# Kernel tuning notes

Hardware: AMD Instinct MI355X
Metric: run time of the kernel (lower is better)

The kernel has to match this reference:

```python
import jax, jax.numpy as jnp
import numpy as np

B, S, MEM, L, E, H = 8, 512, 512, 4, 512, 8
DH = E // H
OBS = 128
K = MEM + S


def setup_inputs() -> dict:
    key = jax.random.key(0)
    ks = jax.random.split(key, 16)
    def w(k, shape, s=0.02):
        return jax.random.normal(k, shape, jnp.float32) * s
    # causal-with-memory mask: query i may attend to kv positions j <= MEM + i
    mask = jnp.arange(K)[None, None, None, :] <= (MEM + jnp.arange(S))[None, None, :, None]
    return {
        "obs": w(ks[0], (B, S, OBS), 1.0),
        "memories": w(ks[1], (B, MEM, L, E), 1.0),
        "mask": mask,
        "W_enc": w(ks[2], (OBS, E)), "b_enc": jnp.zeros((E,), jnp.float32),
        "ln1_s": jnp.ones((L, E), jnp.float32), "ln1_b": jnp.zeros((L, E), jnp.float32),
        "Wq": w(ks[3], (L, E, H, DH)), "bq": jnp.zeros((L, H, DH), jnp.float32),
        "Wk": w(ks[4], (L, E, H, DH)), "bk": jnp.zeros((L, H, DH), jnp.float32),
        "Wv": w(ks[5], (L, E, H, DH)), "bv": jnp.zeros((L, H, DH), jnp.float32),
        "Wr": w(ks[6], (L, E, H, DH)),
        "u_bias": w(ks[7], (L, H, DH)), "v_bias": w(ks[8], (L, H, DH)),
        "Wo": w(ks[9], (L, H, DH, E)), "bo": jnp.zeros((L, E), jnp.float32),
        "ln2_s": jnp.ones((L, E), jnp.float32), "ln2_b": jnp.zeros((L, E), jnp.float32),
        "W1": w(ks[10], (L, E, E)), "b1": jnp.zeros((L, E), jnp.float32),
        "W2": w(ks[11], (L, E, E)), "b2": jnp.zeros((L, E), jnp.float32),
    }


def _ln(x, s, b, eps=1e-6):
    m = x.mean(-1, keepdims=True)
    v = ((x - m) ** 2).mean(-1, keepdims=True)
    return (x - m) * jax.lax.rsqrt(v + eps) * s + b


def _rel_shift(x):
    # Transformer-XL relative shift: [B,H,Q,Kk] -> shifted [B,H,Q,Kk]
    b, h, q, k = x.shape
    x = jnp.pad(x, ((0, 0), (0, 0), (0, 0), (1, 0)))
    return x.reshape(b, h, k + 1, q)[:, :, 1:, :].reshape(b, h, q, k)


def _forward(obs, memories, mask, W_enc, b_enc, ln1_s, ln1_b, Wq, bq, Wk, bk, Wv, bv,
             Wr, u_bias, v_bias, Wo, bo, ln2_s, ln2_b, W1, b1, W2, b2):
    x = obs @ W_enc + b_enc  # [B,S,E]
    klen = memories.shape[1] + x.shape[1]
    e = x.shape[-1]
    # PositionalEmbedding: pos_seq = [klen, klen-1, ..., 1]
    inv_freq = 1.0 / (10000.0 ** (jnp.arange(0, e, 2, dtype=jnp.float32) / e))
    sin_inp = jnp.outer(jnp.arange(klen, 0, -1, dtype=jnp.float32), inv_freq)
    pe = jnp.concatenate([jnp.sin(sin_inp), jnp.cos(sin_inp)], axis=-1)  # [K,E]
    scale = 1.0 / jnp.sqrt(jnp.asarray(Wq.shape[-1], jnp.float32))
    for i in range(Wq.shape[0]):
        mem_cat = jnp.concatenate([memories[:, :, i], x], axis=1)  # [B,K,E]
        vk = _ln(mem_cat, ln1_s[i], ln1_b[i])
        qn = _ln(x, ln1_s[i], ln1_b[i])
        q = jnp.einsum('bse,ehd->bshd', qn, Wq[i]) + bq[i]
        k = jnp.einsum('bke,ehd->bkhd', vk, Wk[i]) + bk[i]
        vv = jnp.einsum('bke,ehd->bkhd', vk, Wv[i]) + bv[i]
        r = jnp.einsum('ke,ehd->khd', pe, Wr[i])
        ac = jnp.einsum('bqhd,bkhd->bhqk', q + u_bias[i], k)     # content term
        bd = _rel_shift(jnp.einsum('bqhd,khd->bhqk', q + v_bias[i], r))  # position term
        scores = jnp.where(mask, (ac + bd) * scale, jnp.float32(-1e30))
        attn = jax.nn.softmax(scores, axis=-1)
        o = jnp.einsum('bhqk,bkhd->bqhd', attn, vv)
        attn_out = jnp.einsum('bqhd,hde->bqe', o, Wo[i]) + bo[i]
        h = x + attn_out                      # residual (gating=False)
        hn = _ln(h, ln2_s[i], ln2_b[i])
        ff = jax.nn.gelu(hn @ W1[i] + b1[i]) @ W2[i] + b2[i]
        x = ff + h
    return x


def reference(obs, memories, mask, W_enc, b_enc, ln1_s, ln1_b, Wq, bq, Wk, bk, Wv, bv,
              Wr, u_bias, v_bias, Wo, bo, ln2_s, ln2_b, W1, b1, W2, b2):
    return _forward(obs, memories, mask, W_enc, b_enc, ln1_s, ln1_b, Wq, bq, Wk, bk,
                    Wv, bv, Wr, u_bias, v_bias, Wo, bo, ln2_s, ln2_b, W1, b1, W2, b2)
```

## Files before the change

### kernel.cpp

```cpp
#include <hip/hip_runtime.h>
#include <hip/hip_bf16.h>
#include <math.h>

#define B     8
#define S     512
#define MEM   512
#define L     4
#define E     512
#define H     8
#define DH    64
#define OBS   128
#define KLEN  1024
#define FQ    64
#define FK    64

typedef __hip_bfloat16 bf16;
using frag_ab = __attribute__((ext_vector_type(8))) short;
using frag_cd = __attribute__((ext_vector_type(4))) float;

__device__ __forceinline__ float gelu_tanh(float x) {
    return 0.5f * x * (1.0f + tanhf(0.7978845608028654f * (x + 0.044715f * x * x * x)));
}
__device__ __forceinline__ unsigned short f2bs(float x) {
    bf16 h = __float2bfloat16(x); return *(unsigned short*)&h;
}
__device__ __forceinline__ float bs2f(short s) {
    union { unsigned u; float f; } t; t.u = ((unsigned)(unsigned short)s) << 16; return t.f;
}

__global__ __launch_bounds__(256) void setup_kernel(
    const float* __restrict__ obs, bf16* __restrict__ obsb, bf16* __restrict__ pe)
{
    const int i = blockIdx.x * 256 + threadIdx.x;
    if (i < B * S * OBS) {
        obsb[i] = __float2bfloat16(obs[i]);
    } else {
        const int idx = i - B * S * OBS;
        const int p = idx >> 9;
        const int j = idx & 511;
        const float pos = (float)(KLEN - p);
        const int m = (j < 256) ? j : (j - 256);
        const float invf = expf(-(float)(2 * m) * (9.210340371976184f / (float)E));
        const float a = pos * invf;
        pe[idx] = __float2bfloat16((j < 256) ? sinf(a) : cosf(a));
    }
}

__global__ __launch_bounds__(256) void transpose_all_kernel(
    const float* __restrict__ Wq, const float* __restrict__ Wk,
    const float* __restrict__ Wv, const float* __restrict__ Wr,
    const float* __restrict__ Wo, const float* __restrict__ W1,
    const float* __restrict__ W2, const float* __restrict__ Wenc,
    bf16* __restrict__ WqT, bf16* __restrict__ WkvT, bf16* __restrict__ WrT,
    bf16* __restrict__ WoT, bf16* __restrict__ W1T, bf16* __restrict__ W2T,
    bf16* __restrict__ WencT)
{
    __shared__ float t[32][33];
    const int z = blockIdx.z;
    const int bn = blockIdx.x * 32, bk = blockIdx.y * 32;
    const int tx = threadIdx.x & 31, ty = threadIdx.x >> 5;
    if (z == 28) {
        if (blockIdx.y >= OBS / 32) return;
        #pragma unroll
        for (int r = 0; r < 32; r += 8)
            t[ty + r][tx] = Wenc[(size_t)(bk + ty + r) * E + bn + tx];
        __syncthreads();
        #pragma unroll
        for (int r = 0; r < 32; r += 8)
            WencT[(size_t)(bn + ty + r) * OBS + bk + tx] = __float2bfloat16(t[tx][ty + r]);
        return;
    }
    const int which = z >> 2, li = z & 3;
    const size_t so = (size_t)li * E * E;
    const float* src; bf16* dst;
    switch (which) {
        case 0: src = Wq + so; dst = WqT + so; break;
        case 1: src = Wk + so; dst = WkvT + (size_t)li * 2 * E * E; break;
        case 2: src = Wv + so; dst = WkvT + (size_t)li * 2 * E * E + (size_t)E * E; break;
        case 3: src = Wr + so; dst = WrT + so; break;
        case 4: src = Wo + so; dst = WoT + so; break;
        case 5: src = W1 + so; dst = W1T + so; break;
        default: src = W2 + so; dst = W2T + so; break;
    }
    #pragma unroll
    for (int r = 0; r < 32; r += 8)
        t[ty + r][tx] = src[(size_t)(bk + ty + r) * E + bn + tx];
    __syncthreads();
    #pragma unroll
    for (int r = 0; r < 32; r += 8)
        dst[(size_t)(bn + ty + r) * E + bk + tx] = __float2bfloat16(t[tx][ty + r]);
}

__device__ __forceinline__ void gemm_body(
    short* As, short* Bs,
    const bf16* __restrict__ A, const bf16* __restrict__ Bt,
    int m0, int n0, int K, int N,
    const float* bias, const float* bias_u, const float* bias_v,
    const float* res, float* Cf, bf16* Cb, bf16* Cb2, int act, int mode)
{
    const int tid = threadIdx.x;
    const int w = tid >> 6, lane = tid & 63;
    const int wm2 = (w >> 1) * 64, wn2 = (w & 1) * 32;
    const int fr = lane & 15, quad = lane >> 4;

    const int arow = tid >> 1, acol = (tid & 1) * 32;
    const int brow = tid >> 2, bcol = (tid & 3) * 16;
    const short* Ag = (const short*)A + (size_t)(m0 + arow) * K + acol;
    const short* Bg = (const short*)Bt + (size_t)(n0 + brow) * K + bcol;
    short* Asw = &As[arow * 72 + acol];
    short* Bsw = &Bs[brow * 72 + bcol];

    frag_cd acc[4][2];
    #pragma unroll
    for (int i = 0; i < 4; ++i)
        #pragma unroll
        for (int j = 0; j < 2; ++j)
            acc[i][j] = (frag_cd)(0.0f);

    uint4 a0 = *(const uint4*)(Ag);
    uint4 a1 = *(const uint4*)(Ag + 8);
    uint4 a2 = *(const uint4*)(Ag + 16);
    uint4 a3 = *(const uint4*)(Ag + 24);
    uint4 b0 = *(const uint4*)(Bg);
    uint4 b1 = *(const uint4*)(Bg + 8);

    for (int k0 = 0; k0 < K; k0 += 64) {
        __syncthreads();
        *(uint4*)(Asw) = a0; *(uint4*)(Asw + 8) = a1;
        *(uint4*)(Asw + 16) = a2; *(uint4*)(Asw + 24) = a3;
        *(uint4*)(Bsw) = b0; *(uint4*)(Bsw + 8) = b1;
        if (k0 + 64 < K) {
            a0 = *(const uint4*)(Ag + k0 + 64);
            a1 = *(const uint4*)(Ag + k0 + 72);
            a2 = *(const uint4*)(Ag + k0 + 80);
            a3 = *(const uint4*)(Ag + k0 + 88);
            b0 = *(const uint4*)(Bg + k0 + 64);
            b1 = *(const uint4*)(Bg + k0 + 72);
        }
        asm volatile("s_waitcnt lgkmcnt(0)" ::: "memory");
        __builtin_amdgcn_s_barrier();
        __builtin_amdgcn_sched_barrier(0);
        #pragma unroll
        for (int kh = 0; kh < 2; ++kh) {
            frag_ab af[4], bfr[2];
            #pragma unroll
            for (int i = 0; i < 4; ++i)
                af[i] = *(const frag_ab*)&As[(wm2 + i * 16 + fr) * 72 + kh * 32 + quad * 8];
            #pragma unroll
            for (int j = 0; j < 2; ++j)
                bfr[j] = *(const frag_ab*)&Bs[(wn2 + j * 16 + fr) * 72 + kh * 32 + quad * 8];
            #pragma unroll
            for (int i = 0; i < 4; ++i)
                #pragma unroll
                for (int j = 0; j < 2; ++j)
                    acc[i][j] = __builtin_amdgcn_mfma_f32_16x16x32_bf16(af[i], bfr[j], acc[i][j], 0, 0, 0);
        }
    }

    if (mode == 2 && n0 >= 512) {
        short* ts = As;
        __syncthreads();
        #pragma unroll
        for (int i = 0; i < 4; ++i) {
            #pragma unroll
            for (int r = 0; r < 4; ++r) {
                const int kl = wm2 + i * 16 + quad * 4 + r;
                #pragma unroll
                for (int j = 0; j < 2; ++j) {
                    const int dl = wn2 + j * 16 + fr;
                    ts[dl * 130 + kl] =
                        (short)f2bs(acc[i][j][r] + bias_v[(n0 - 512) + dl]);
                }
            }
        }
        __syncthreads();
        const int bb = m0 >> 10;
        const int kb = m0 & 1023;
        const int dl = tid >> 2;
        const int q4 = tid & 3;
        short vals[32];
        #pragma unroll
        for (int i2 = 0; i2 < 32; ++i2) {
            const int kp  = q4 * 32 + i2;
            const int kpl = kp & 63;
            const int src = (kp & 64) + (((kpl & 3) << 4) | (kpl >> 2));
            vals[i2] = ts[dl * 130 + src];
        }
        short* dst = (short*)Cb2 + ((size_t)(bb * E + (n0 - 512) + dl)) * KLEN
                   + kb + q4 * 32;
        *(uint4*)(dst)      = *(const uint4*)&vals[0];
        *(uint4*)(dst + 8)  = *(const uint4*)&vals[8];
        *(uint4*)(dst + 16) = *(const uint4*)&vals[16];
        *(uint4*)(dst + 24) = *(const uint4*)&vals[24];
        return;
    }

    #pragma unroll
    for (int i = 0; i < 4; ++i) {
        #pragma unroll
        for (int r = 0; r < 4; ++r) {
            const int m = m0 + wm2 + i * 16 + quad * 4 + r;
            #pragma unroll
            for (int j = 0; j < 2; ++j) {
                const int n = n0 + wn2 + j * 16 + fr;
                float v = acc[i][j][r];
                if (bias) v += bias[n];
                if (act)  v = gelu_tanh(v);
                if (res)  v += res[(size_t)m * N + n];
                if (mode == 2) {
                    Cb[(size_t)m * 512 + n] = __float2bfloat16(v + bias_u[n]);
                } else if (mode == 1) {
                    Cb[(size_t)m * N + n]  = __float2bfloat16((v + bias_u[n]) * 0.125f);
                    Cb2[(size_t)m * N + n] = __float2bfloat16((v + bias_v[n]) * 0.125f);
                } else {
                    if (Cf) Cf[(size_t)m * N + n] = v;
                    if (Cb) Cb[(size_t)m * N + n] = __float2bfloat16(v);
                }
            }
        }
    }
}

__device__ __forceinline__ void gemm64_body(
    short* As, short* Bs,
    const bf16* __restrict__ A, const bf16* __restrict__ Bt,
    int m0, int n0, int K, int N,
    const float* bias, const float* res, float* Cf, bf16* Cb, int act)
{
    const int tid = threadIdx.x;
    const int w = tid >> 6, lane = tid & 63;
    const int wm2 = (w >> 1) * 32, wn2 = (w & 1) * 32;
    const int fr = lane & 15, quad = lane >> 4;

    const int arow = tid >> 2, acol = (tid & 3) * 16;
    const short* Ag = (const short*)A + (size_t)(m0 + arow) * K + acol;
    const short* Bg = (const short*)Bt + (size_t)(n0 + arow) * K + acol;
    short* Asw = &As[arow * 72 + acol];
    short* Bsw = &Bs[arow * 72 + acol];

    frag_cd acc[2][2];
    #pragma unroll
    for (int i = 0; i < 2; ++i)
        #pragma unroll
        for (int j = 0; j < 2; ++j)
            acc[i][j] = (frag_cd)(0.0f);

    uint4 a0 = *(const uint4*)(Ag);
    uint4 a1 = *(const uint4*)(Ag + 8);
    uint4 b0 = *(const uint4*)(Bg);
    uint4 b1 = *(const uint4*)(Bg + 8);

    for (int k0 = 0; k0 < K; k0 += 64) {
        __syncthreads();
        *(uint4*)(Asw) = a0; *(uint4*)(Asw + 8) = a1;
        *(uint4*)(Bsw) = b0; *(uint4*)(Bsw + 8) = b1;
        if (k0 + 64 < K) {
            a0 = *(const uint4*)(Ag + k0 + 64);
            a1 = *(const uint4*)(Ag + k0 + 72);
            b0 = *(const uint4*)(Bg + k0 + 64);
            b1 = *(const uint4*)(Bg + k0 + 72);
        }
        asm volatile("s_waitcnt lgkmcnt(0)" ::: "memory");
        __builtin_amdgcn_s_barrier();
        __builtin_amdgcn_sched_barrier(0);
        #pragma unroll
        for (int kh = 0; kh < 2; ++kh) {
            frag_ab af[2], bfr[2];
            #pragma unroll
            for (int i = 0; i < 2; ++i)
                af[i] = *(const frag_ab*)&As[(wm2 + i * 16 + fr) * 72 + kh * 32 + quad * 8];
            #pragma unroll
            for (int j = 0; j < 2; ++j)
                bfr[j] = *(const frag_ab*)&Bs[(wn2 + j * 16 + fr) * 72 + kh * 32 + quad * 8];
            #pragma unroll
            for (int i = 0; i < 2; ++i)
                #pragma unroll
                for (int j = 0; j < 2; ++j)
                    acc[i][j] = __builtin_amdgcn_mfma_f32_16x16x32_bf16(af[i], bfr[j], acc[i][j], 0, 0, 0);
        }
    }

    #pragma unroll
    for (int i = 0; i < 2; ++i) {
        #pragma unroll
        for (int r = 0; r < 4; ++r) {
            const int m = m0 + wm2 + i * 16 + quad * 4 + r;
            #pragma unroll
            for (int j = 0; j < 2; ++j) {
                const int n = n0 + wn2 + j * 16 + fr;
                float v = acc[i][j][r];
                if (bias) v += bias[n];
                if (act)  v = gelu_tanh(v);
                if (res)  v += res[(size_t)m * N + n];
                if (Cf) Cf[(size_t)m * N + n] = v;
                if (Cb) Cb[(size_t)m * N + n] = __float2bfloat16(v);
            }
        }
    }
}

__global__ __launch_bounds__(256) void mfma_gemm_kernel(
    const bf16* __restrict__ A, const bf16* __restrict__ Bt,
    const float* __restrict__ bias, const float* __restrict__ res,
    float* __restrict__ Cf, bf16* __restrict__ Cb,
    int K, int N, int act)
{
    __shared__ short As[64 * 72];
    __shared__ short Bs[64 * 72];
    const int pid = blockIdx.x;
    const int swz = ((pid & 7) << 6) | (pid >> 3);
    gemm64_body(As, Bs, A, Bt, (swz >> 3) * 64, (swz & 7) * 64, K, N,
                bias, res, Cf, Cb, act);
}

__global__ __launch_bounds__(256) void qkvr_kernel(
    const bf16* __restrict__ QN, const bf16* __restrict__ VK,
    const bf16* __restrict__ PE_, const bf16* __restrict__ WqT,
    const bf16* __restrict__ WkvT, const bf16* __restrict__ WrT,
    const float* __restrict__ bq, const float* __restrict__ ub,
    const float* __restrict__ vbias, const float* __restrict__ bk,
    const float* __restrict__ bv,
    bf16* __restrict__ QU, bf16* __restrict__ QV,
    bf16* __restrict__ KB, bf16* __restrict__ VT, bf16* __restrict__ RB)
{
    __shared__ short As[128 * 72];
    __shared__ short Bs[64 * 72];
    const int bid = blockIdx.x;
    if (bid < 256) {
        const int swz = ((bid & 7) << 5) | (bid >> 3);
        gemm_body(As, Bs, QN, WqT, (swz >> 3) * 128, (swz & 7) * 64, E, E,
                  bq, ub, vbias, nullptr, nullptr, QU, QV, 0, 1);
    } else if (bid < 1280) {
        const int id = bid - 256;
        const int swz = ((id & 7) << 7) | (id >> 3);
        gemm_body(As, Bs, VK, WkvT, (swz >> 4) * 128, (swz & 15) * 64, E, 2 * E,
                  nullptr, bk, bv, nullptr, nullptr, KB, VT, 0, 2);
    } else {
        const int id = bid - 1280;
        const int swz = ((id & 7) << 3) | (id >> 3);
        gemm_body(As, Bs, PE_, WrT, (swz >> 3) * 128, (swz & 7) * 64, E, E,
                  nullptr, nullptr, nullptr, nullptr, nullptr, RB, nullptr, 0, 0);
    }
}

__global__ __launch_bounds__(256) void ln1_kernel(
    const float* __restrict__ mem, const float* __restrict__ X, int li,
    const float* __restrict__ gam, const float* __restrict__ bet,
    bf16* __restrict__ qn, bf16* __restrict__ vkdst)
{
    const int blk = blockIdx.x;
    const int t = threadIdx.x;
    const bool isMem = blk < B * MEM;
    const int rr = isMem ? blk : (blk - B * MEM);
    const float* sp = isMem ? (mem + ((size_t)rr * L + li) * E)
                            : (X + (size_t)rr * E);
    const float x0 = sp[t], x1 = sp[t + 256];
    float s = x0 + x1, ss = fmaf(x0, x0, x1 * x1);
    #pragma unroll
    for (int off = 32; off; off >>= 1) { s += __shfl_down(s, off, 64); ss += __shfl_down(ss, off, 64); }
    __shared__ float tmp[8];
    const int wid = t >> 6, lane = t & 63;
    if (!lane) { tmp[wid] = s; tmp[4 + wid] = ss; }
    __syncthreads();
    s = tmp[0] + tmp[1] + tmp[2] + tmp[3];
    ss = tmp[4] + tmp[5] + tmp[6] + tmp[7];
    const float mean = s * (1.0f / E);
    const float var = ss * (1.0f / E) - mean * mean;
    const float rstd = rsqrtf(var + 1e-6f);
    const float y0 = (x0 - mean) * rstd * gam[t] + bet[t];
    const float y1 = (x1 - mean) * rstd * gam[t + 256] + bet[t + 256];
    const int b = rr >> 9, p = rr & 511;
    if (isMem) {
        bf16* dst = vkdst + ((size_t)b * KLEN + p) * E;
        dst[t] = __float2bfloat16(y0); dst[t + 256] = __float2bfloat16(y1);
    } else {
        qn[(size_t)rr * E + t]       = __float2bfloat16(y0);
        qn[(size_t)rr * E + t + 256] = __float2bfloat16(y1);
        bf16* d2 = vkdst + ((size_t)b * KLEN + MEM + p) * E;
        d2[t] = __float2bfloat16(y0); d2[t + 256] = __float2bfloat16(y1);
    }
}

__global__ __launch_bounds__(256) void ln_f32_kernel(
    const float* __restrict__ src,
    const float* __restrict__ gam, const float* __restrict__ bet,
    bf16* __restrict__ dst1)
{
    const int rr = blockIdx.x;
    const int t = threadIdx.x;
    const float* sp = src + (size_t)rr * E;
    const float x0 = sp[t], x1 = sp[t + 256];
    float s = x0 + x1, ss = fmaf(x0, x0, x1 * x1);
    #pragma unroll
    for (int off = 32; off; off >>= 1) { s += __shfl_down(s, off, 64); ss += __shfl_down(ss, off, 64); }
    __shared__ float tmp[8];
    const int wid = t >> 6, lane = t & 63;
    if (!lane) { tmp[wid] = s; tmp[4 + wid] = ss; }
    __syncthreads();
    s = tmp[0] + tmp[1] + tmp[2] + tmp[3];
    ss = tmp[4] + tmp[5] + tmp[6] + tmp[7];
    const float mean = s * (1.0f / E);
    const float var = ss * (1.0f / E) - mean * mean;
    const float rstd = rsqrtf(var + 1e-6f);
    dst1[(size_t)rr * E + t]       = __float2bfloat16((x0 - mean) * rstd * gam[t] + bet[t]);
    dst1[(size_t)rr * E + t + 256] = __float2bfloat16((x1 - mean) * rstd * gam[t + 256] + bet[t + 256]);
}

__global__ __launch_bounds__(256) void mfma_flash_kernel(
    const bf16* __restrict__ Qu,
    const bf16* __restrict__ Qv,
    const bf16* __restrict__ Kb,
    const bf16* __restrict__ Vt,
    const bf16* __restrict__ Rb,
    bf16* __restrict__ O)
{
    const int pid = blockIdx.x;
    const int swz = ((pid & 7) << 6) | (pid >> 3);
    const int qphys = swz & 7;
    const int hb = swz >> 3;
    const int h = hb & 7, b = hb >> 3;
    const int qt = (qphys & 1) ? (7 - (qphys >> 1)) : (qphys >> 1);
    const int q0 = qt * FQ;
    const int t = threadIdx.x;
    const int w = t >> 6, lane = t & 63;
    const int fr = lane & 15, quad = lane >> 4;
    const int qbase = q0 + w * 16;

    __shared__ short Ks[64 * 64];
    __shared__ short Vs[64 * 64];
    __shared__ short Rs[128 * 64];
    __shared__ short BDs[4 * 80 * 18];
    __shared__ short Ps[4 * 16 * 64];

    const int fxk = fr & 7;
    const int xq0 = (quad ^ fxk) << 3;
    const int xq1 = ((quad + 4) ^ fxk) << 3;

    const short* quptr = (const short*)Qu + ((size_t)(b * S + qbase + fr)) * E + h * DH + quad * 8;
    const frag_ab au0 = *(const frag_ab*)(quptr);
    const frag_ab au1 = *(const frag_ab*)(quptr + 32);
    const short* qvptr = (const short*)Qv + ((size_t)(b * S + qbase + fr)) * E + h * DH + quad * 8;
    const frag_ab av0 = *(const frag_ab*)(qvptr);
    const frag_ab av1 = *(const frag_ab*)(qvptr + 32);

    frag_cd accO[4];
    #pragma unroll
    for (int i = 0; i < 4; ++i) accO[i] = (frag_cd)(0.0f);
    float mrow[4] = {-3.0e38f, -3.0e38f, -3.0e38f, -3.0e38f};
    float lrow[4] = {0.f, 0.f, 0.f, 0.f};

    const int srow = t >> 2, scol = (t & 3) * 16;
    const short* kg = (const short*)Kb + ((size_t)(b * KLEN + srow)) * E + h * DH + scol;
    const short* vg = (const short*)Vt + ((size_t)(b * E + h * DH + srow)) * KLEN + scol;
    const int sxs = srow & 7;
    const int scb = (t & 3) * 2;
    const int kvw0 = (srow << 6) + (((scb    ) ^ sxs) << 3);
    const int kvw1 = (srow << 6) + (((scb + 1) ^ sxs) << 3);
    const int ntb0 = 3 - w;
    const int b0 = 448 - q0;

    {
        const int rr = t >> 1, rc = (t & 1) * 32;
        const int j = b0 + rr;
        const int slot = j & 127;
        const int sx = slot & 7, cb = rc >> 3;
        const short* rp = (const short*)Rb + (size_t)j * E + h * DH + rc;
        *(uint4*)&Rs[(slot << 6) + (((cb    ) ^ sx) << 3)] = *(const uint4*)(rp);
        *(uint4*)&Rs[(slot << 6) + (((cb + 1) ^ sx) << 3)] = *(const uint4*)(rp + 8);
        *(uint4*)&Rs[(slot << 6) + (((cb + 2) ^ sx) << 3)] = *(const uint4*)(rp + 16);
        *(uint4*)&Rs[(slot << 6) + (((cb + 3) ^ sx) << 3)] = *(const uint4*)(rp + 24);
    }

    const int ntiles = 9 + qt;

    const int r64 = t >> 2, rc4 = (t & 3) * 16;
    uint4 ka0, ka1, va0, va1, ra0, ra1;
    int rslot = 0;
    {
        ka0 = *(const uint4*)(kg);
        ka1 = *(const uint4*)(kg + 8);
        va0 = *(const uint4*)(vg);
        va1 = *(const uint4*)(vg + 8);
    }

    for (int kt = 0; kt < ntiles; ++kt) {
        const int k0 = kt * FK;
        __syncthreads();
        {
            *(uint4*)&Ks[kvw0] = ka0;
            *(uint4*)&Ks[kvw1] = ka1;
            *(uint4*)&Vs[kvw0] = va0;
            *(uint4*)&Vs[kvw1] = va1;
        }
        if (kt >= 1) {
            const int sx = rslot & 7;
            *(uint4*)&Rs[(rslot << 6) + (((scb    ) ^ sx) << 3)] = ra0;
            *(uint4*)&Rs[(rslot << 6) + (((scb + 1) ^ sx) << 3)] = ra1;
        }
        if (kt + 1 < ntiles) {
            const short* kp = kg + (size_t)(k0 + FK) * E;
            ka0 = *(const uint4*)(kp);
            ka1 = *(const uint4*)(kp + 8);
            const short* vp = vg + k0 + FK;
            va0 = *(const uint4*)(vp);
            va1 = *(const uint4*)(vp + 8);
            int j = b0 + 64 * (kt + 1) + 64 + r64;
            rslot = j & 127;
            if (j > KLEN - 1) j = KLEN - 1;
            const short* rp = (const short*)Rb + (size_t)j * E + h * DH + rc4;
            ra0 = *(const uint4*)(rp);
            ra1 = *(const uint4*)(rp + 8);
        }
        asm volatile("s_waitcnt lgkmcnt(0)" ::: "memory");
        __builtin_amdgcn_s_barrier();
        __builtin_amdgcn_sched_barrier(0);

        const int roff = (b0 + 64 * kt) & 127;

        __builtin_amdgcn_s_setprio(1);
        #pragma unroll
        for (int i = 0; i < 5; ++i) {
            const int ntb = ntb0 + i;
            const int slot = (roff + ntb * 16 + fr) & 127;
            const frag_ab rf0 = *(const frag_ab*)&Rs[(slot << 6) + xq0];
            const frag_ab rf1 = *(const frag_ab*)&Rs[(slot << 6) + xq1];
            frag_cd z = (frag_cd)(0.0f);
            z = __builtin_amdgcn_mfma_f32_16x16x32_bf16(av0, rf0, z, 0, 0, 0);
            z = __builtin_amdgcn_mfma_f32_16x16x32_bf16(av1, rf1, z, 0, 0, 0);
            union { unsigned u[2]; unsigned short sh[4]; } pk;
            pk.sh[0] = f2bs(z[0]); pk.sh[1] = f2bs(z[1]);
            pk.sh[2] = f2bs(z[2]); pk.sh[3] = f2bs(z[3]);
            const int bdw = (w * 80 + i * 16 + fr) * 18 + quad * 4;
            *(unsigned*)&BDs[bdw]     = pk.u[0];
            *(unsigned*)&BDs[bdw + 2] = pk.u[1];
        }

        frag_cd sc[4];
        #pragma unroll
        for (int nt = 0; nt < 4; ++nt) {
            const int krow = (nt * 16 + fr) << 6;
            const frag_ab kf0 = *(const frag_ab*)&Ks[krow + xq0];
            const frag_ab kf1 = *(const frag_ab*)&Ks[krow + xq1];
            frag_cd z = (frag_cd)(0.0f);
            z = __builtin_amdgcn_mfma_f32_16x16x32_bf16(au0, kf0, z, 0, 0, 0);
            z = __builtin_amdgcn_mfma_f32_16x16x32_bf16(au1, kf1, z, 0, 0, 0);
            sc[nt] = z;
        }
        __builtin_amdgcn_s_setprio(0);

        const bool edge = (kt == ntiles - 1);
        #pragma unroll
        for (int r = 0; r < 4; ++r) {
            const int qw = quad * 4 + r;
            float sv[4];
            #pragma unroll
            for (int nt = 0; nt < 4; ++nt) {
                const int jlr = nt * 16 + fr + 15 - qw;
                const float bd = bs2f(BDs[(w * 80 + jlr) * 18 + qw]);
                sv[nt] = sc[nt][r] + bd;
            }
            if (edge) {
                const int qrow = qbase + qw;
                #pragma unroll
                for (int nt = 0; nt < 4; ++nt)
                    if (k0 + nt * 16 + fr > MEM + qrow) sv[nt] = -1e30f;
            }
            const float locmax = fmaxf(fmaxf(sv[0], sv[1]), fmaxf(sv[2], sv[3]));
            if (__any(locmax > mrow[r] + 4.0f)) {
                float tm = locmax;
                tm = fmaxf(tm, __shfl_xor(tm, 1, 64));
                tm = fmaxf(tm, __shfl_xor(tm, 2, 64));
                tm = fmaxf(tm, __shfl_xor(tm, 4, 64));
                tm = fmaxf(tm, __shfl_xor(tm, 8, 64));
                const float mn = fmaxf(mrow[r], tm);
                const float al = __expf(mrow[r] - mn);
                lrow[r] *= al;
                #pragma unroll
                for (int nt = 0; nt < 4; ++nt) accO[nt][r] *= al;
                mrow[r] = mn;
            }
            const float p0 = __expf(sv[0] - mrow[r]), p1 = __expf(sv[1] - mrow[r]);
            const float p2 = __expf(sv[2] - mrow[r]), p3 = __expf(sv[3] - mrow[r]);
            lrow[r] += (p0 + p1) + (p2 + p3);
            union { uint2 u2; unsigned short sh[4]; } pq;
            pq.sh[0] = f2bs(p0); pq.sh[1] = f2bs(p1);
            pq.sh[2] = f2bs(p2); pq.sh[3] = f2bs(p3);
            const int pw = (w << 10) + (qw << 6)
                         + (((fr >> 1) ^ (qw & 7)) << 3) + ((fr & 1) << 2);
            *(uint2*)&Ps[pw] = pq.u2;
        }

        const frag_ab pf0 = *(const frag_ab*)&Ps[(w << 10) + (fr << 6) + xq0];
        const frag_ab pf1 = *(const frag_ab*)&Ps[(w << 10) + (fr << 6) + xq1];
        __builtin_amdgcn_s_setprio(1);
        #pragma unroll
        for (int nt = 0; nt < 4; ++nt) {
            const int vrow = (nt * 16 + fr) << 6;
            const frag_ab vf0 = *(const frag_ab*)&Vs[vrow + xq0];
            const frag_ab vf1 = *(const frag_ab*)&Vs[vrow + xq1];
            accO[nt] = __builtin_amdgcn_mfma_f32_16x16x32_bf16(pf0, vf0, accO[nt], 0, 0, 0);
            accO[nt] = __builtin_amdgcn_mfma_f32_16x16x32_bf16(pf1, vf1, accO[nt], 0, 0, 0);
        }
        __builtin_amdgcn_s_setprio(0);
    }

    #pragma unroll
    for (int r = 0; r < 4; ++r) {
        float lsum = lrow[r];
        lsum += __shfl_xor(lsum, 1, 64);
        lsum += __shfl_xor(lsum, 2, 64);
        lsum += __shfl_xor(lsum, 4, 64);
        lsum += __shfl_xor(lsum, 8, 64);
        const float inv = 1.0f / lsum;
        bf16* po = O + ((size_t)(b * S + qbase + quad * 4 + r)) * E + h * DH + fr;
        #pragma unroll
        for (int nt = 0; nt < 4; ++nt)
            po[nt * 16] = __float2bfloat16(accO[nt][r] * inv);
    }
}

extern "C" void kernel_launch(void* const* d_in, const int* in_sizes, int n_in,
                              void* d_out, int out_size, void* d_ws, size_t ws_size,
                              hipStream_t stream)
{
    const float* obs  = (const float*)d_in[0];
    const float* mem  = (const float*)d_in[1];
    const float* Wenc = (const float*)d_in[3];
    const float* benc = (const float*)d_in[4];
    const float* ln1s = (const float*)d_in[5];
    const float* ln1b = (const float*)d_in[6];
    const float* Wq   = (const float*)d_in[7];
    const float* bq   = (const float*)d_in[8];
    const float* Wk   = (const float*)d_in[9];
    const float* bk   = (const float*)d_in[10];
    const float* Wv   = (const float*)d_in[11];
    const float* bv   = (const float*)d_in[12];
    const float* Wr   = (const float*)d_in[13];
    const float* ub   = (const float*)d_in[14];
    const float* vb   = (const float*)d_in[15];
    const float* Wo   = (const float*)d_in[16];
    const float* bo   = (const float*)d_in[17];
    const float* ln2s = (const float*)d_in[18];
    const float* ln2b = (const float*)d_in[19];
    const float* W1   = (const float*)d_in[20];
    const float* b1   = (const float*)d_in[21];
    const float* W2   = (const float*)d_in[22];
    const float* b2   = (const float*)d_in[23];

    float* wsf = (float*)d_ws;
    float* X = wsf;
    bf16* wsb = (bf16*)(wsf + (size_t)B * S * E);
    size_t ob = 0;
    bf16* OBSb = wsb + ob; ob += (size_t)B * S * OBS;
    bf16* QNb  = wsb + ob; ob += (size_t)B * S * E;
    bf16* PEb  = wsb + ob; ob += (size_t)KLEN * E;
    bf16* RBb  = wsb + ob; ob += (size_t)KLEN * E;
    bf16* WencT= wsb + ob; ob += (size_t)OBS * E;
    bf16* WqT  = wsb + ob; ob += (size_t)L * E * E;
    bf16* WkvT = wsb + ob; ob += (size_t)L * 2 * E * E;
    bf16* WrT  = wsb + ob; ob += (size_t)L * E * E;
    bf16* WoT  = wsb + ob; ob += (size_t)L * E * E;
    bf16* W1T  = wsb + ob; ob += (size_t)L * E * E;
    bf16* W2T  = wsb + ob; ob += (size_t)L * E * E;
    bf16* QUb  = wsb + ob; ob += (size_t)B * S * E;
    bf16* QVb  = wsb + ob; ob += (size_t)B * S * E;
    bf16* KBb  = wsb + ob; ob += (size_t)B * KLEN * E;
    bf16* VTb  = wsb + ob; ob += (size_t)B * E * KLEN;
    bf16* OBb  = wsb + ob; ob += (size_t)B * S * E;
    char* uni = (char*)(wsb + ob);
    bf16*  VKb = (bf16*)uni;
    float* HB  = (float*)uni;
    bf16*  FFb = (bf16*)(uni + ((size_t)8 << 20));


    transpose_all_kernel<<<dim3(E / 32, E / 32, 29), 256, 0, stream>>>(
        Wq, Wk, Wv, Wr, Wo, W1, W2, Wenc, WqT, WkvT, WrT, WoT, W1T, W2T, WencT);
    setup_kernel<<<(B * S * OBS + KLEN * E) / 256, 256, 0, stream>>>(obs, OBSb, PEb);

    mfma_gemm_kernel<<<512, 256, 0, stream>>>(
        OBSb, WencT, benc, nullptr, X, nullptr, OBS, E, 0);

    for (int li = 0; li < L; ++li) {
        const size_t wOff = (size_t)li * E * E;
        const size_t vOff = (size_t)li * E;

        ln1_kernel<<<2 * B * S, 256, 0, stream>>>(
            mem, X, li, ln1s + vOff, ln1b + vOff, QNb, VKb);

        qkvr_kernel<<<1344, 256, 0, stream>>>(
            QNb, VKb, PEb, WqT + wOff, WkvT + (size_t)li * 2 * E * E, WrT + wOff,
            bq + vOff, ub + vOff, vb + vOff, bk + vOff, bv + vOff,
            QUb, QVb, KBb, VTb, RBb);

        mfma_flash_kernel<<<512, 256, 0, stream>>>(
            QUb, QVb, KBb, VTb, RBb, OBb);

        mfma_gemm_kernel<<<512, 256, 0, stream>>>(
            OBb, WoT + wOff, bo + vOff, X, HB, nullptr, E, E, 0);
        ln_f32_kernel<<<B * S, 256, 0, stream>>>(HB, ln2s + vOff, ln2b + vOff, QNb);
        mfma_gemm_kernel<<<512, 256, 0, stream>>>(
            QNb, W1T + wOff, b1 + vOff, nullptr, nullptr, FFb, E, E, 1);
        float* dst = (li == L - 1) ? (float*)d_out : X;
        mfma_gemm_kernel<<<512, 256, 0, stream>>>(
            FFb, W2T + wOff, b2 + vOff, HB, dst, nullptr, E, E, 0);
    }
}
```

Baseline: 614.8 us.

## Fuse LayerNorm2 into Wo GEMM stats epilogue and W1 GEMM prologue

The Wo projection GEMM epilogue now accumulates per-row sum and sum-of-squares into a stats buffer via atomics, and a new W1 GEMM kernel applies the LayerNorm on the fly while loading f32 activations into shared memory. This removes the standalone ln_f32 kernel and its bf16 intermediate write/read each layer. Costs are atomic traffic, reading f32 instead of bf16 for the W1 A operand, and stats zeroing piggybacked on ln1_kernel. Variance is computed as E[x^2]-mean^2, which has slightly different numerics.

Result: faster. 580.9 us (median of 2 runs) (-5.5%).

```diff
diff --git a/kernel.cpp b/kernel.cpp
--- a/kernel.cpp
+++ b/kernel.cpp
@@ -225,7 +225,8 @@
     short* As, short* Bs,
     const bf16* __restrict__ A, const bf16* __restrict__ Bt,
     int m0, int n0, int K, int N,
-    const float* bias, const float* res, float* Cf, bf16* Cb, int act)
+    const float* bias, const float* res, float* Cf, bf16* Cb, int act,
+    float* stats)
 {
     const int tid = threadIdx.x;
     const int w = tid >> 6, lane = tid & 63;
@@ -285,6 +286,7 @@
         #pragma unroll
         for (int r = 0; r < 4; ++r) {
             const int m = m0 + wm2 + i * 16 + quad * 4 + r;
+            float s = 0.0f, sq = 0.0f;
             #pragma unroll
             for (int j = 0; j < 2; ++j) {
                 const int n = n0 + wn2 + j * 16 + fr;
@@ -294,6 +296,17 @@
                 if (res)  v += res[(size_t)m * N + n];
                 if (Cf) Cf[(size_t)m * N + n] = v;
                 if (Cb) Cb[(size_t)m * N + n] = __float2bfloat16(v);
+                s += v; sq = fmaf(v, v, sq);
+            }
+            if (stats) {
+                s  += __shfl_xor(s, 1, 64);  sq += __shfl_xor(sq, 1, 64);
+                s  += __shfl_xor(s, 2, 64);  sq += __shfl_xor(sq, 2, 64);
+                s  += __shfl_xor(s, 4, 64);  sq += __shfl_xor(sq, 4, 64);
+                s  += __shfl_xor(s, 8, 64);  sq += __shfl_xor(sq, 8, 64);
+                if (fr == 0) {
+                    atomicAdd(&stats[2 * m], s);
+                    atomicAdd(&stats[2 * m + 1], sq);
+                }
             }
         }
     }
@@ -303,14 +316,126 @@
     const bf16* __restrict__ A, const bf16* __restrict__ Bt,
     const float* __restrict__ bias, const float* __restrict__ res,
     float* __restrict__ Cf, bf16* __restrict__ Cb,
-    int K, int N, int act)
+    int K, int N, int act, float* stats)
 {
     __shared__ short As[64 * 72];
     __shared__ short Bs[64 * 72];
     const int pid = blockIdx.x;
     const int swz = ((pid & 7) << 6) | (pid >> 3);
     gemm64_body(As, Bs, A, Bt, (swz >> 3) * 64, (swz & 7) * 64, K, N,
-                bias, res, Cf, Cb, act);
+                bias, res, Cf, Cb, act, stats);
+}
+
+__global__ __launch_bounds__(256) void mfma_gemm_ln_kernel(
+    const float* __restrict__ A, const bf16* __restrict__ Bt,
+    const float* __restrict__ ST,
+    const float* __restrict__ gam, const float* __restrict__ bet,
+    const float* __restrict__ bias, bf16* __restrict__ Cb)
+{
+    __shared__ short As[64 * 72];
+    __shared__ short Bs[64 * 72];
+    __shared__ float gls[E], bls[E];
+    const int pid = blockIdx.x;
+    const int swz = ((pid & 7) << 6) | (pid >> 3);
+    const int m0 = (swz >> 3) * 64, n0 = (swz & 7) * 64;
+    const int tid = threadIdx.x;
+    *(float2*)&gls[tid * 2] = *(const float2*)&gam[tid * 2];
+    *(float2*)&bls[tid * 2] = *(const float2*)&bet[tid * 2];
+
+    const int w = tid >> 6, lane = tid & 63;
+    const int wm2 = (w >> 1) * 32, wn2 = (w & 1) * 32;
+    const int fr = lane & 15, quad = lane >> 4;
+
+    const int arow = tid >> 2, acol = (tid & 3) * 16;
+    const int g = m0 + arow;
+    const float mean = ST[2 * g] * (1.0f / E);
+    const float var  = ST[2 * g + 1] * (1.0f / E) - mean * mean;
+    const float rstd = rsqrtf(var + 1e-6f);
+    const float* Agf = A + (size_t)g * E + acol;
+    const short* Bg = (const short*)Bt + (size_t)(n0 + arow) * E + acol;
+    short* Asw = &As[arow * 72 + acol];
+    short* Bsw = &Bs[arow * 72 + acol];
+
+    frag_cd acc[2][2];
+    #pragma unroll
+    for (int i = 0; i < 2; ++i)
+        #pragma unroll
+        for (int j = 0; j < 2; ++j)
+            acc[i][j] = (frag_cd)(0.0f);
+
+    float4 f0 = *(const float4*)(Agf);
+    float4 f1 = *(const float4*)(Agf + 4);
+    float4 f2 = *(const float4*)(Agf + 8);
+    float4 f3 = *(const float4*)(Agf + 12);
+    uint4 b0 = *(const uint4*)(Bg);
+    uint4 b1 = *(const uint4*)(Bg + 8);
+
+    for (int k0 = 0; k0 < E; k0 += 64) {
+        __syncthreads();
+        {
+            const float* gp = &gls[k0 + acol];
+            const float* bp = &bls[k0 + acol];
+            union { uint4 u; unsigned short s[8]; } p0, p1;
+            p0.s[0] = f2bs((f0.x - mean) * rstd * gp[0]  + bp[0]);
+            p0.s[1] = f2bs((f0.y - mean) * rstd * gp[1]  + bp[1]);
+            p0.s[2] = f2bs((f0.z - mean) * rstd * gp[2]  + bp[2]);
+            p0.s[3] = f2bs((f0.w - mean) * rstd * gp[3]  + bp[3]);
+            p0.s[4] = f2bs((f1.x - mean) * rstd * gp[4]  + bp[4]);
+            p0.s[5] = f2bs((f1.y - mean) * rstd * gp[5]  + bp[5]);
+            p0.s[6] = f2bs((f1.z - mean) * rstd * gp[6]  + bp[6]);
+            p0.s[7] = f2bs((f1.w - mean) * rstd * gp[7]  + bp[7]);
+            p1.s[0] = f2bs((f2.x - mean) * rstd * gp[8]  + bp[8]);
+            p1.s[1] = f2bs((f2.y - mean) * rstd * gp[9]  + bp[9]);
+            p1.s[2] = f2bs((f2.z - mean) * rstd * gp[10] + bp[10]);
+            p1.s[3] = f2bs((f2.w - mean) * rstd * gp[11] + bp[11]);
+            p1.s[4] = f2bs((f3.x - mean) * rstd * gp[12] + bp[12]);
+            p1.s[5] = f2bs((f3.y - mean) * rstd * gp[13] + bp[13]);
+            p1.s[6] = f2bs((f3.z - mean) * rstd * gp[14] + bp[14]);
+            p1.s[7] = f2bs((f3.w - mean) * rstd * gp[15] + bp[15]);
+            *(uint4*)(Asw) = p0.u; *(uint4*)(Asw + 8) = p1.u;
+        }
+        *(uint4*)(Bsw) = b0; *(uint4*)(Bsw + 8) = b1;
+        if (k0 + 64 < E) {
+            f0 = *(const float4*)(Agf + k0 + 64);
+            f1 = *(const float4*)(Agf + k0 + 68);
+            f2 = *(const float4*)(Agf + k0 + 72);
+            f3 = *(const float4*)(Agf + k0 + 76);
+            b0 = *(const uint4*)(Bg + k0 + 64);
+            b1 = *(const uint4*)(Bg + k0 + 72);
+        }
+        asm volatile("s_waitcnt lgkmcnt(0)" ::: "memory");
+        __builtin_amdgcn_s_barrier();
+        __builtin_amdgcn_sched_barrier(0);
+        #pragma unroll
+        for (int kh = 0; kh < 2; ++kh) {
+            frag_ab af[2], bfr[2];
+            #pragma unroll
+            for (int i = 0; i < 2; ++i)
+                af[i] = *(const frag_ab*)&As[(wm2 + i * 16 + fr) * 72 + kh * 32 + quad * 8];
+            #pragma unroll
+            for (int j = 0; j < 2; ++j)
+                bfr[j] = *(const frag_ab*)&Bs[(wn2 + j * 16 + fr) * 72 + kh * 32 + quad * 8];
+            #pragma unroll
+            for (int i = 0; i < 2; ++i)
+                #pragma unroll
+                for (int j = 0; j < 2; ++j)
+                    acc[i][j] = __builtin_amdgcn_mfma_f32_16x16x32_bf16(af[i], bfr[j], acc[i][j], 0, 0, 0);
+        }
+    }
+
+    #pragma unroll
+    for (int i = 0; i < 2; ++i) {
+        #pragma unroll
+        for (int r = 0; r < 4; ++r) {
+            const int m = m0 + wm2 + i * 16 + quad * 4 + r;
+            #pragma unroll
+            for (int j = 0; j < 2; ++j) {
+                const int n = n0 + wn2 + j * 16 + fr;
+                const float v = gelu_tanh(acc[i][j][r] + bias[n]);
+                Cb[(size_t)m * E + n] = __float2bfloat16(v);
+            }
+        }
+    }
 }
 
 __global__ __launch_bounds__(256) void qkvr_kernel(
@@ -346,10 +471,11 @@
 __global__ __launch_bounds__(256) void ln1_kernel(
     const float* __restrict__ mem, const float* __restrict__ X, int li,
     const float* __restrict__ gam, const float* __restrict__ bet,
-    bf16* __restrict__ qn, bf16* __restrict__ vkdst)
+    bf16* __restrict__ qn, bf16* __restrict__ vkdst, float* __restrict__ st)
 {
     const int blk = blockIdx.x;
     const int t = threadIdx.x;
+    if (blk < 32) st[blk * 256 + t] = 0.0f;
     const bool isMem = blk < B * MEM;
     const int rr = isMem ? blk : (blk - B * MEM);
     const float* sp = isMem ? (mem + ((size_t)rr * L + li) * E)
@@ -379,31 +505,6 @@
         bf16* d2 = vkdst + ((size_t)b * KLEN + MEM + p) * E;
         d2[t] = __float2bfloat16(y0); d2[t + 256] = __float2bfloat16(y1);
     }
-}
-
-__global__ __launch_bounds__(256) void ln_f32_kernel(
-    const float* __restrict__ src,
-    const float* __restrict__ gam, const float* __restrict__ bet,
-    bf16* __restrict__ dst1)
-{
-    const int rr = blockIdx.x;
-    const int t = threadIdx.x;
-    const float* sp = src + (size_t)rr * E;
-    const float x0 = sp[t], x1 = sp[t + 256];
-    float s = x0 + x1, ss = fmaf(x0, x0, x1 * x1);
-    #pragma unroll
-    for (int off = 32; off; off >>= 1) { s += __shfl_down(s, off, 64); ss += __shfl_down(ss, off, 64); }
-    __shared__ float tmp[8];
-    const int wid = t >> 6, lane = t & 63;
-    if (!lane) { tmp[wid] = s; tmp[4 + wid] = ss; }
-    __syncthreads();
-    s = tmp[0] + tmp[1] + tmp[2] + tmp[3];
-    ss = tmp[4] + tmp[5] + tmp[6] + tmp[7];
-    const float mean = s * (1.0f / E);
-    const float var = ss * (1.0f / E) - mean * mean;
-    const float rstd = rsqrtf(var + 1e-6f);
-    dst1[(size_t)rr * E + t]       = __float2bfloat16((x0 - mean) * rstd * gam[t] + bet[t]);
-    dst1[(size_t)rr * E + t + 256] = __float2bfloat16((x1 - mean) * rstd * gam[t + 256] + bet[t + 256]);
 }
 
 __global__ __launch_bounds__(256) void mfma_flash_kernel(
@@ -667,6 +768,7 @@
     bf16* KBb  = wsb + ob; ob += (size_t)B * KLEN * E;
     bf16* VTb  = wsb + ob; ob += (size_t)B * E * KLEN;
     bf16* OBb  = wsb + ob; ob += (size_t)B * S * E;
+    float* ST  = (float*)(wsb + ob); ob += 16384;
     char* uni = (char*)(wsb + ob);
     bf16*  VKb = (bf16*)uni;
     float* HB  = (float*)uni;
@@ -678,14 +780,14 @@
     setup_kernel<<<(B * S * OBS + KLEN * E) / 256, 256, 0, stream>>>(obs, OBSb, PEb);
 
     mfma_gemm_kernel<<<512, 256, 0, stream>>>(
-        OBSb, WencT, benc, nullptr, X, nullptr, OBS, E, 0);
+        OBSb, WencT, benc, nullptr, X, nullptr, OBS, E, 0, nullptr);
 
     for (int li = 0; li < L; ++li) {
         const size_t wOff = (size_t)li * E * E;
         const size_t vOff = (size_t)li * E;
 
         ln1_kernel<<<2 * B * S, 256, 0, stream>>>(
-            mem, X, li, ln1s + vOff, ln1b + vOff, QNb, VKb);
+            mem, X, li, ln1s + vOff, ln1b + vOff, QNb, VKb, ST);
 
         qkvr_kernel<<<1344, 256, 0, stream>>>(
             QNb, VKb, PEb, WqT + wOff, WkvT + (size_t)li * 2 * E * E, WrT + wOff,
@@ -696,12 +798,11 @@
             QUb, QVb, KBb, VTb, RBb, OBb);
 
         mfma_gemm_kernel<<<512, 256, 0, stream>>>(
-            OBb, WoT + wOff, bo + vOff, X, HB, nullptr, E, E, 0);
-        ln_f32_kernel<<<B * S, 256, 0, stream>>>(HB, ln2s + vOff, ln2b + vOff, QNb);
-        mfma_gemm_kernel<<<512, 256, 0, stream>>>(
-            QNb, W1T + wOff, b1 + vOff, nullptr, nullptr, FFb, E, E, 1);
+            OBb, WoT + wOff, bo + vOff, X, HB, nullptr, E, E, 0, ST);
+        mfma_gemm_ln_kernel<<<512, 256, 0, stream>>>(
+            HB, W1T + wOff, ST, ln2s + vOff, ln2b + vOff, b1 + vOff, FFb);
         float* dst = (li == L - 1) ? (float*)d_out : X;
         mfma_gemm_kernel<<<512, 256, 0, stream>>>(
-            FFb, W2T + wOff, b2 + vOff, HB, dst, nullptr, E, E, 0);
-    }
-}
+            FFb, W2T + wOff, b2 + vOff, HB, dst, nullptr, E, E, 0, nullptr);
+    }
+}
```
